# Kernel tuning notes

Hardware: AMD Instinct MI355X
Metric: run time of the kernel (lower is better)

Reference implementation:

```python
import jax, jax.numpy as jnp
import numpy as np

N, E, IN, HID, H, C, L, NC = 10000, 60000, 768, 256, 8, 256, 4, 2
EPS, SLOPE = 1e-5, 0.2

def _ln(x, g, b):
    m = x.mean(-1, keepdims=True)
    v = x.var(-1, keepdims=True)
    return (x - m) / jnp.sqrt(v + EPS) * g + b

def _gelu(x):
    return jax.nn.gelu(x, approximate=False)  # torch nn.GELU default (erf)

def setup_inputs() -> dict:
    key = jax.random.key(0)
    ks = iter(jax.random.split(key, 40))
    def p(shape, s=0.02):
        return jax.random.normal(next(ks), shape, jnp.float32) * s
    return dict(
        x=jax.random.normal(next(ks), (N, IN), jnp.float32),
        edge_index=jax.random.randint(next(ks), (2, E), 0, N, dtype=jnp.int32),
        W_in=p((HID, IN)), b_in=jnp.zeros((HID,), jnp.float32),
        virtual_node=p((1, HID)),
        Wl=p((L, H * C, HID)), bl=jnp.zeros((L, H * C), jnp.float32),
        Wr=p((L, H * C, HID)), br=jnp.zeros((L, H * C), jnp.float32),
        att=p((L, H, C)), gbias=jnp.zeros((L, HID), jnp.float32),
        V1=p((L, 2 * HID, HID)), v1b=jnp.zeros((L, 2 * HID), jnp.float32),
        V2=p((L, HID, 2 * HID)), v2b=jnp.zeros((L, HID), jnp.float32),
        U1=p((L, 2 * HID, 2 * HID)), u1b=jnp.zeros((L, 2 * HID), jnp.float32),
        U2=p((L, HID, 2 * HID)), u2b=jnp.zeros((L, HID), jnp.float32),
        g1=jnp.ones((L, HID), jnp.float32), be1=jnp.zeros((L, HID), jnp.float32),
        g2=jnp.ones((L, HID), jnp.float32), be2=jnp.zeros((L, HID), jnp.float32),
        g3=jnp.ones((L, HID), jnp.float32), be3=jnp.zeros((L, HID), jnp.float32),
        O1=p((HID, HID)), o1b=jnp.zeros((HID,), jnp.float32),
        O2=p((NC, HID)), o2b=jnp.zeros((NC,), jnp.float32),
    )

def reference(x, edge_index, W_in, b_in, virtual_node, Wl, bl, Wr, br, att, gbias,
              V1, v1b, V2, v2b, U1, u1b, U2, u2b,
              g1, be1, g2, be2, g3, be3, O1, o1b, O2, o2b):
    # add self loops (PyG add_self_loops=True)
    loops = jnp.arange(N, dtype=edge_index.dtype)
    src = jnp.concatenate([edge_index[0], loops])  # message sources j
    dst = jnp.concatenate([edge_index[1], loops])  # message targets i

    x = x @ W_in.T + b_in                      # [N, HID]
    vn = virtual_node                          # [1, HID]
    for i in range(L):
        # --- GATv2Conv (concat=False -> mean over heads), eval mode (no dropout) ---
        xl = (x @ Wl[i].T + bl[i]).reshape(N, H, C)   # source transform
        xr = (x @ Wr[i].T + br[i]).reshape(N, H, C)   # target transform
        m = jax.nn.leaky_relu(xl[src] + xr[dst], SLOPE)       # [Etot, H, C]
        e = jnp.einsum('ehc,hc->eh', m, att[i])                # [Etot, H]
        emax = jax.ops.segment_max(e, dst, num_segments=N)
        a = jnp.exp(e - emax[dst])
        denom = jax.ops.segment_sum(a, dst, num_segments=N)
        alpha = a / denom[dst]                                  # segment softmax
        agg = jax.ops.segment_sum(xl[src] * alpha[:, :, None], dst, num_segments=N)
        x_local = agg.mean(axis=1) + gbias[i]                   # [N, HID]
        x = _ln(x + x_local, g1[i], be1[i])
        # --- virtual node update ---
        vn_in = x.mean(axis=0, keepdims=True)
        vn_up = _gelu(vn_in @ V1[i].T + v1b[i]) @ V2[i].T + v2b[i]
        vn = _ln(vn + vn_up, g2[i], be2[i])
        # --- node update with broadcast VN ---
        xc = jnp.concatenate([x, jnp.broadcast_to(vn, (N, HID))], axis=1)
        xu = _gelu(xc @ U1[i].T + u1b[i]) @ U2[i].T + u2b[i]
        x = _ln(x + xu, g3[i], be3[i])
    return _gelu(x @ O1.T + o1b) @ O2.T + o2b
```

## Files before the change

### kernel.cpp

```cpp
#include <hip/hip_runtime.h>
#include <hip/hip_bf16.h>
#include <cstdint>
#include <cstddef>

#define N_NODES 10000
#define M_PAD   10112
#define N_EDGES 60000
#define ETOT    70000
#define DIM_IN  768
#define HID     256
#define NHEAD   8
#define CH      256
#define HC      2048
#define NLAYER  4
#define NCLS    2
#define EPSLN   1e-5f
#define SLOPE   0.2f
#define DEG_CAP 128

typedef __bf16 bf16;
typedef __bf16 bf16x8 __attribute__((ext_vector_type(8)));
typedef float  f32x4  __attribute__((ext_vector_type(4)));

__device__ __forceinline__ float gelu_erf(float x) {
  return 0.5f * x * (1.0f + erff(x * 0.70710678118654752f));
}

__device__ __forceinline__ void gl2lds16(const void* g, void* l) {
  __builtin_amdgcn_global_load_lds(
      (const __attribute__((address_space(1))) unsigned int*)g,
      (__attribute__((address_space(3))) unsigned int*)l,
      16, 0, 0);
}

__global__ void k_count(const int* __restrict__ ei, int* __restrict__ deg) {
  int e = blockIdx.x * 256 + threadIdx.x;
  if (e >= ETOT) return;
  int d = (e < N_EDGES) ? ei[N_EDGES + e] : (e - N_EDGES);
  atomicAdd(&deg[d], 1);
}

__global__ void k_scan(const int* __restrict__ deg, int* __restrict__ offs) {
  __shared__ int lds[1024];
  const int t = threadIdx.x;
  const int c0 = t * 10;
  int s = 0;
  #pragma unroll
  for (int q = 0; q < 10; ++q) { int idx = c0 + q; if (idx < N_NODES) s += deg[idx]; }
  lds[t] = s;
  __syncthreads();
  for (int o = 1; o < 1024; o <<= 1) {
    int v = (t >= o) ? lds[t - o] : 0;
    __syncthreads();
    lds[t] += v;
    __syncthreads();
  }
  int run = lds[t] - s;
  #pragma unroll
  for (int q = 0; q < 10; ++q) {
    int idx = c0 + q;
    if (idx < N_NODES) { offs[idx] = run; run += deg[idx]; }
  }
  if (t == 1023) offs[N_NODES] = lds[1023];
}

__global__ void k_scatter(const int* __restrict__ ei, const int* __restrict__ offs,
                          int* __restrict__ fill, int* __restrict__ adj) {
  int e = blockIdx.x * 256 + threadIdx.x;
  if (e >= ETOT) return;
  int s, d;
  if (e < N_EDGES) { s = ei[e]; d = ei[N_EDGES + e]; } else { s = e - N_EDGES; d = s; }
  int pos = offs[d] + atomicAdd(&fill[d], 1);
  adj[pos] = s;
}

__global__ void k_init_vn(const float* __restrict__ vnode, float* __restrict__ vn_cur) {
  int t = threadIdx.x;
  if (t < HID) vn_cur[t] = vnode[t];
}

__global__ void k_f2b(const float* __restrict__ src, bf16* __restrict__ dst, int n4) {
  int i = blockIdx.x * 256 + threadIdx.x;
  int stride = gridDim.x * 256;
  for (; i < n4; i += stride) {
    float4 v = reinterpret_cast<const float4*>(src)[i];
    bf16 o0 = (bf16)v.x, o1 = (bf16)v.y, o2 = (bf16)v.z, o3 = (bf16)v.w;
    ushort4 pack;
    pack.x = __builtin_bit_cast(unsigned short, o0);
    pack.y = __builtin_bit_cast(unsigned short, o1);
    pack.z = __builtin_bit_cast(unsigned short, o2);
    pack.w = __builtin_bit_cast(unsigned short, o3);
    reinterpret_cast<ushort4*>(dst)[i] = pack;
  }
}

__global__ void k_catw(const float* __restrict__ Wl, const float* __restrict__ Wr,
                       bf16* __restrict__ out) {
  int idx = blockIdx.x * 256 + threadIdx.x;
  const int total8 = NLAYER * 4096 * 256 / 8;
  if (idx >= total8) return;
  size_t flat = (size_t)idx * 8;
  int i   = (int)(flat / (4096 * 256));
  int rem = (int)(flat % (4096 * 256));
  int r = rem >> 8;
  int k = rem & 255;
  const float* src = (r < 2048)
      ? Wl + (((size_t)i * 2048 + r) << 8) + k
      : Wr + (((size_t)i * 2048 + (r - 2048)) << 8) + k;
  const float4* p4 = reinterpret_cast<const float4*>(src);
  float4 u0 = p4[0], u1 = p4[1];
  bf16x8 ov;
  ov[0]=(bf16)u0.x; ov[1]=(bf16)u0.y; ov[2]=(bf16)u0.z; ov[3]=(bf16)u0.w;
  ov[4]=(bf16)u1.x; ov[5]=(bf16)u1.y; ov[6]=(bf16)u1.z; ov[7]=(bf16)u1.w;
  reinterpret_cast<bf16x8*>(out)[idx] = ov;
}

__global__ void k_catb(const float* __restrict__ bl, const float* __restrict__ br,
                       float* __restrict__ out) {
  int idx = blockIdx.x * 256 + threadIdx.x;
  if (idx >= NLAYER * 4096) return;
  int i = idx >> 12, r = idx & 4095;
  out[idx] = (r < 2048) ? bl[i * 2048 + r] : br[i * 2048 + (r - 2048)];
}

template<int ACT, bool WB, bool WF>
__global__ __launch_bounds__(256) void k_gemm2(
    const bf16* __restrict__ A, int lda,
    const bf16* __restrict__ W, int ldw,
    const float* __restrict__ bias,
    bf16* __restrict__ Cb, float* __restrict__ Cf, int ldc,
    int M, int K)
{
  __shared__ bf16 As[128 * 64];
  __shared__ bf16 Bs[128 * 64];
  const int t = threadIdx.x;
  const int bm = blockIdx.x * 128;
  const int bn = blockIdx.y * 128;
  const int l = t & 63, w = t >> 6;
  const int wm = (w >> 1) * 64, wn = (w & 1) * 64;
  const int lr = l & 15, lg = l >> 4;
  const int sr = t >> 3;
  const int ps = t & 7;

  f32x4 acc[4][4];
  #pragma unroll
  for (int a = 0; a < 4; ++a)
    #pragma unroll
    for (int b = 0; b < 4; ++b) acc[a][b] = (f32x4){0.f, 0.f, 0.f, 0.f};

  for (int k0 = 0; k0 < K; k0 += 64) {
    #pragma unroll
    for (int q = 0; q < 4; ++q) {
      int r = q * 32 + sr;
      int ls = ps ^ (r & 7);
      gl2lds16(A + (size_t)(bm + r) * lda + k0 + ls * 8, &As[r * 64 + ps * 8]);
    }
    #pragma unroll
    for (int q = 0; q < 4; ++q) {
      int r = q * 32 + sr;
      int ls = ps ^ (r & 7);
      gl2lds16(W + (size_t)(bn + r) * ldw + k0 + ls * 8, &Bs[r * 64 + ps * 8]);
    }
    __syncthreads();
    #pragma unroll
    for (int ks = 0; ks < 2; ++ks) {
      bf16x8 af[4], bfr[4];
      #pragma unroll
      for (int mt = 0; mt < 4; ++mt) {
        int row = wm + mt * 16 + lr;
        int slot = ks * 4 + lg;
        af[mt] = *reinterpret_cast<const bf16x8*>(&As[row * 64 + ((slot ^ (row & 7)) * 8)]);
      }
      #pragma unroll
      for (int nt = 0; nt < 4; ++nt) {
        int row = wn + nt * 16 + lr;
        int slot = ks * 4 + lg;
        bfr[nt] = *reinterpret_cast<const bf16x8*>(&Bs[row * 64 + ((slot ^ (row & 7)) * 8)]);
      }
      #pragma unroll
      for (int mt = 0; mt < 4; ++mt)
        #pragma unroll
        for (int nt = 0; nt < 4; ++nt)
          acc[mt][nt] = __builtin_amdgcn_mfma_f32_16x16x32_bf16(af[mt], bfr[nt], acc[mt][nt], 0, 0, 0);
    }
    __syncthreads();
  }
  #pragma unroll
  for (int mt = 0; mt < 4; ++mt) {
    #pragma unroll
    for (int nt = 0; nt < 4; ++nt) {
      int col = bn + wn + nt * 16 + lr;
      float bv = bias[col];
      #pragma unroll
      for (int j = 0; j < 4; ++j) {
        int row = bm + wm + mt * 16 + lg * 4 + j;
        if (row < M) {
          float vv = acc[mt][nt][j] + bv;
          if (ACT == 1) vv = gelu_erf(vv);
          if (WB) Cb[(size_t)row * ldc + col] = (bf16)vv;
          if (WF) Cf[(size_t)row * ldc + col] = vv;
        }
      }
    }
  }
}

__global__ __launch_bounds__(256) void k_node_attn(
    float* __restrict__ x, bf16* __restrict__ xb,
    const bf16* __restrict__ xlr,
    const int* __restrict__ offs, const int* __restrict__ adj,
    const float* __restrict__ att_l, const float* __restrict__ gbias_l,
    const float* __restrict__ g_l, const float* __restrict__ b_l)
{
  __shared__ int   s_src[DEG_CAP];
  __shared__ float s_agg[HC];
  __shared__ float s_red[8];

  const int t = threadIdx.x;
  const int i = blockIdx.x;
  const int start = offs[i];
  int deg = offs[i + 1] - start;
  if (deg > DEG_CAP) deg = DEG_CAP;

  for (int j = t; j < deg; j += 256) s_src[j] = adj[start + j];

  float xr_reg[8], att_reg[8];
  {
    bf16x8 xv = *reinterpret_cast<const bf16x8*>(xlr + (size_t)i * 4096 + 2048 + 8 * t);
    #pragma unroll
    for (int q = 0; q < 8; ++q) xr_reg[q] = (float)xv[q];
    const float4* ap = reinterpret_cast<const float4*>(att_l + 8 * t);
    float4 a0 = ap[0], a1 = ap[1];
    att_reg[0]=a0.x; att_reg[1]=a0.y; att_reg[2]=a0.z; att_reg[3]=a0.w;
    att_reg[4]=a1.x; att_reg[5]=a1.y; att_reg[6]=a1.z; att_reg[7]=a1.w;
  }
  __syncthreads();

  float m = -1e30f, ssum = 0.f;
  float acc[8];
  #pragma unroll
  for (int q = 0; q < 8; ++q) acc[q] = 0.f;

  for (int j = 0; j < deg; ++j) {
    bf16x8 xv = *reinterpret_cast<const bf16x8*>(xlr + (size_t)s_src[j] * 4096 + 8 * t);
    float xf[8];
    float p = 0.f;
    #pragma unroll
    for (int q = 0; q < 8; ++q) {
      xf[q] = (float)xv[q];
      float z = xf[q] + xr_reg[q];
      z = (z > 0.f) ? z : SLOPE * z;
      p = fmaf(att_reg[q], z, p);
    }
    #pragma unroll
    for (int o = 16; o >= 1; o >>= 1) p += __shfl_xor(p, o, 32);
    if (__any(p > m)) {
      float mn = fmaxf(m, p);
      float scale = __expf(m - mn);
      ssum *= scale;
      #pragma unroll
      for (int q = 0; q < 8; ++q) acc[q] *= scale;
      m = mn;
    }
    float a = __expf(p - m);
    ssum += a;
    #pragma unroll
    for (int q = 0; q < 8; ++q) acc[q] = fmaf(a, xf[q], acc[q]);
  }
  float inv = 1.0f / ssum;
  #pragma unroll
  for (int q = 0; q < 8; ++q) s_agg[8 * t + q] = acc[q] * inv;
  __syncthreads();

  float xloc = 0.f;
  #pragma unroll
  for (int hh = 0; hh < NHEAD; ++hh) xloc += s_agg[hh * CH + t];
  xloc = xloc * (1.0f / NHEAD) + gbias_l[t];
  float r = x[(size_t)i * HID + t] + xloc;

  float s1 = r, s2 = r * r;
  #pragma unroll
  for (int o = 32; o >= 1; o >>= 1) { s1 += __shfl_xor(s1, o); s2 += __shfl_xor(s2, o); }
  if ((t & 63) == 0) { s_red[t >> 6] = s1; s_red[4 + (t >> 6)] = s2; }
  __syncthreads();
  s1 = s_red[0] + s_red[1] + s_red[2] + s_red[3];
  s2 = s_red[4] + s_red[5] + s_red[6] + s_red[7];
  float mean = s1 * (1.0f / HID);
  float var  = s2 * (1.0f / HID) - mean * mean;
  float o = (r - mean) * rsqrtf(var + EPSLN) * g_l[t] + b_l[t];
  x [(size_t)i * HID + t] = o;
  xb[(size_t)i * HID + t] = (bf16)o;
}

__global__ void k_colmean(const float* __restrict__ x, float* __restrict__ accum) {
  const int t = threadIdx.x, b = blockIdx.x;
  float s = 0.f;
  for (int r = b * 50; r < (b + 1) * 50; ++r) s += x[(size_t)r * HID + t];
  atomicAdd(&accum[t], s);
}

__global__ void k_vn_gemv1(const float* __restrict__ vn_accum,
                           const float* __restrict__ V1, const float* __restrict__ v1b,
                           float* __restrict__ z1) {
  const int o = blockIdx.x * 8 + (threadIdx.x >> 5);
  const int lane = threadIdx.x & 31;
  const float4* vp = reinterpret_cast<const float4*>(vn_accum + lane * 8);
  float4 a0 = vp[0], a1 = vp[1];
  const float4* wp = reinterpret_cast<const float4*>(V1 + (size_t)o * 256 + lane * 8);
  float4 w0 = wp[0], w1 = wp[1];
  float p = a0.x*w0.x + a0.y*w0.y + a0.z*w0.z + a0.w*w0.w
          + a1.x*w1.x + a1.y*w1.y + a1.z*w1.z + a1.w*w1.w;
  #pragma unroll
  for (int s = 16; s >= 1; s >>= 1) p += __shfl_xor(p, s, 32);
  if (lane == 0) z1[o] = gelu_erf(p * (1.0f / (float)N_NODES) + v1b[o]);
}

__global__ void k_vn_gemv2(const float* __restrict__ z1,
                           const float* __restrict__ V2, const float* __restrict__ v2b,
                           float* __restrict__ vn_up) {
  const int o = blockIdx.x * 8 + (threadIdx.x >> 5);
  const int lane = threadIdx.x & 31;
  float p = 0.f;
  #pragma unroll
  for (int c = 0; c < 4; ++c) {
    float4 a = reinterpret_cast<const float4*>(z1 + lane * 16)[c];
    float4 w = reinterpret_cast<const float4*>(V2 + (size_t)o * 512 + lane * 16)[c];
    p += a.x*w.x + a.y*w.y + a.z*w.z + a.w*w.w;
  }
  #pragma unroll
  for (int s = 16; s >= 1; s >>= 1) p += __shfl_xor(p, s, 32);
  if (lane == 0) vn_up[o] = p + v2b[o];
}

__global__ void k_vn_ln(float* __restrict__ vn_cur, const float* __restrict__ vn_up,
                        const float* __restrict__ g2, const float* __restrict__ be2) {
  __shared__ float s_red[8];
  const int t = threadIdx.x;
  float r = vn_cur[t] + vn_up[t];
  float s1 = r, s2 = r * r;
  #pragma unroll
  for (int o = 32; o >= 1; o >>= 1) { s1 += __shfl_xor(s1, o); s2 += __shfl_xor(s2, o); }
  if ((t & 63) == 0) { s_red[t >> 6] = s1; s_red[4 + (t >> 6)] = s2; }
  __syncthreads();
  s1 = s_red[0] + s_red[1] + s_red[2] + s_red[3];
  s2 = s_red[4] + s_red[5] + s_red[6] + s_red[7];
  float mean = s1 * (1.0f / HID);
  float var  = s2 * (1.0f / HID) - mean * mean;
  vn_cur[t] = (r - mean) * rsqrtf(var + EPSLN) * g2[t] + be2[t];
}

__global__ void k_vn_ctr(const float* __restrict__ vn_cur,
                         const float* __restrict__ U1, const float* __restrict__ u1b,
                         float* __restrict__ vn_ctr) {
  const int o = blockIdx.x * 8 + (threadIdx.x >> 5);
  const int lane = threadIdx.x & 31;
  const float4* vp = reinterpret_cast<const float4*>(vn_cur + lane * 8);
  float4 a0 = vp[0], a1 = vp[1];
  const float4* wp = reinterpret_cast<const float4*>(U1 + (size_t)o * 512 + 256 + lane * 8);
  float4 w0 = wp[0], w1 = wp[1];
  float p = a0.x*w0.x + a0.y*w0.y + a0.z*w0.z + a0.w*w0.w
          + a1.x*w1.x + a1.y*w1.y + a1.z*w1.z + a1.w*w1.w;
  #pragma unroll
  for (int s = 16; s >= 1; s >>= 1) p += __shfl_xor(p, s, 32);
  if (lane == 0) vn_ctr[o] = p + u1b[o];
}

__global__ __launch_bounds__(256) void k_ln_res(
    float* __restrict__ x, bf16* __restrict__ xb, const float* __restrict__ xu,
    const float* __restrict__ g_l, const float* __restrict__ b_l)
{
  __shared__ float s_red[8];
  const int t = threadIdx.x, i = blockIdx.x;
  float r = x[(size_t)i * HID + t] + xu[(size_t)i * HID + t];
  float s1 = r, s2 = r * r;
  #pragma unroll
  for (int o = 32; o >= 1; o >>= 1) { s1 += __shfl_xor(s1, o); s2 += __shfl_xor(s2, o); }
  if ((t & 63) == 0) { s_red[t >> 6] = s1; s_red[4 + (t >> 6)] = s2; }
  __syncthreads();
  s1 = s_red[0] + s_red[1] + s_red[2] + s_red[3];
  s2 = s_red[4] + s_red[5] + s_red[6] + s_red[7];
  float mean = s1 * (1.0f / HID);
  float var  = s2 * (1.0f / HID) - mean * mean;
  float o = (r - mean) * rsqrtf(var + EPSLN) * g_l[t] + b_l[t];
  x [(size_t)i * HID + t] = o;
  xb[(size_t)i * HID + t] = (bf16)o;
}

__global__ void k_final(const float* __restrict__ g, const float* __restrict__ O2,
                        const float* __restrict__ o2b, float* __restrict__ out) {
  int tid = blockIdx.x * 256 + threadIdx.x;
  if (tid >= N_NODES * NCLS) return;
  int n = tid >> 1, j = tid & 1;
  const float* gr = g + (size_t)n * HID;
  const float* w  = O2 + (size_t)j * HID;
  float d = o2b[j];
  for (int k = 0; k < HID; ++k) d = fmaf(gr[k], w[k], d);
  out[tid] = d;
}

extern "C" void kernel_launch(void* const* d_in, const int* in_sizes, int n_in,
                              void* d_out, int out_size, void* d_ws, size_t ws_size,
                              hipStream_t stream)
{
  const float* x_in  = (const float*)d_in[0];
  const int*   ei    = (const int*)  d_in[1];
  const float* W_in  = (const float*)d_in[2];
  const float* b_in  = (const float*)d_in[3];
  const float* vnode = (const float*)d_in[4];
  const float* Wl    = (const float*)d_in[5];
  const float* bl    = (const float*)d_in[6];
  const float* Wr    = (const float*)d_in[7];
  const float* br    = (const float*)d_in[8];
  const float* att   = (const float*)d_in[9];
  const float* gbias = (const float*)d_in[10];
  const float* V1    = (const float*)d_in[11];
  const float* v1b   = (const float*)d_in[12];
  const float* V2    = (const float*)d_in[13];
  const float* v2b   = (const float*)d_in[14];
  const float* U1    = (const float*)d_in[15];
  const float* u1b   = (const float*)d_in[16];
  const float* U2    = (const float*)d_in[17];
  const float* u2b   = (const float*)d_in[18];
  const float* g1    = (const float*)d_in[19];
  const float* be1   = (const float*)d_in[20];
  const float* g2    = (const float*)d_in[21];
  const float* be2   = (const float*)d_in[22];
  const float* g3    = (const float*)d_in[23];
  const float* be3   = (const float*)d_in[24];
  const float* O1    = (const float*)d_in[25];
  const float* o1b   = (const float*)d_in[26];
  const float* O2    = (const float*)d_in[27];
  const float* o2b   = (const float*)d_in[28];
  float* out = (float*)d_out;

  char* ws = (char*)d_ws;
  size_t cur = 0;
  auto alloc = [&](size_t bytes) -> char* {
    char* p = ws + cur;
    cur = (cur + bytes + 255) & ~(size_t)255;
    return p;
  };
  float* x        = (float*)alloc((size_t)M_PAD * HID * 4);
  bf16*  xb       = (bf16*) alloc((size_t)M_PAD * HID * 2);
  bf16*  xlr      = (bf16*) alloc((size_t)M_PAD * 4096 * 2);
  bf16*  h1       = (bf16*) alloc((size_t)M_PAD * 2 * HID * 2);
  float* xu       = (float*)alloc((size_t)M_PAD * HID * 4);
  bf16*  Wlrb     = (bf16*) alloc((size_t)NLAYER * 4096 * HID * 2);
  float* blr      = (float*)alloc((size_t)NLAYER * 4096 * 4);
  bf16*  U1b      = (bf16*) alloc((size_t)NLAYER * 2 * HID * 2 * HID * 2);
  bf16*  U2b      = (bf16*) alloc((size_t)NLAYER * HID * 2 * HID * 2);
  bf16*  O1b      = (bf16*) alloc((size_t)HID * HID * 2);
  bf16*  Winb     = (bf16*) alloc((size_t)HID * DIM_IN * 2);
  int*   deg      = (int*)  alloc((size_t)N_NODES * 4);
  int*   offs     = (int*)  alloc((size_t)(N_NODES + 1) * 4);
  int*   fill     = (int*)  alloc((size_t)N_NODES * 4);
  int*   adj      = (int*)  alloc((size_t)ETOT * 4);
  float* vn_accum = (float*)alloc(HID * 4);
  float* vn_cur   = (float*)alloc(HID * 4);
  float* vn_ctr   = (float*)alloc(2 * HID * 4);
  float* z1buf    = (float*)alloc(2 * HID * 4);
  float* vn_up    = (float*)alloc(HID * 4);

  bf16* x_in_b = xlr;

  hipMemsetAsync(deg, 0, (size_t)N_NODES * 4, stream);
  hipMemsetAsync(fill, 0, (size_t)N_NODES * 4, stream);
  k_count<<<(ETOT + 255) / 256, 256, 0, stream>>>(ei, deg);
  k_scan<<<1, 1024, 0, stream>>>(deg, offs);
  k_scatter<<<(ETOT + 255) / 256, 256, 0, stream>>>(ei, offs, fill, adj);
  k_init_vn<<<1, 256, 0, stream>>>(vnode, vn_cur);

  k_catw<<<(NLAYER * 4096 * 256 / 8 + 255) / 256, 256, 0, stream>>>(Wl, Wr, Wlrb);
  k_catb<<<(NLAYER * 4096 + 255) / 256, 256, 0, stream>>>(bl, br, blr);
  k_f2b<<<256, 256, 0, stream>>>(U1, U1b, NLAYER * 2 * HID * 2 * HID / 4);
  k_f2b<<<128, 256, 0, stream>>>(U2, U2b, NLAYER * HID * 2 * HID / 4);
  k_f2b<<<64, 256, 0, stream>>>(O1, O1b, HID * HID / 4);
  k_f2b<<<64, 256, 0, stream>>>(W_in, Winb, HID * DIM_IN / 4);
  k_f2b<<<512, 256, 0, stream>>>(x_in, x_in_b, N_NODES * DIM_IN / 4);

  {
    dim3 g(M_PAD / 128, HID / 128);
    k_gemm2<0, true, true><<<g, 256, 0, stream>>>(
        x_in_b, DIM_IN, Winb, DIM_IN, b_in, xb, x, HID, N_NODES, DIM_IN);
  }

  dim3 g_proj(M_PAD / 128, 4096 / 128);
  dim3 g_u1  (M_PAD / 128, (2 * HID) / 128);
  dim3 g_u2  (M_PAD / 128, HID / 128);

  for (int i = 0; i < NLAYER; ++i) {
    const bf16* Wlrb_i = Wlrb + (size_t)i * 4096 * HID;
    const bf16* U1b_i  = U1b + (size_t)i * 2 * HID * 2 * HID;
    const bf16* U2b_i  = U2b + (size_t)i * HID * 2 * HID;

    k_gemm2<0, true, false><<<g_proj, 256, 0, stream>>>(
        xb, HID, Wlrb_i, HID, blr + (size_t)i * 4096, xlr, nullptr, 4096, N_NODES, HID);

    k_node_attn<<<N_NODES, 256, 0, stream>>>(x, xb, xlr, offs, adj,
        att + (size_t)i * HC, gbias + (size_t)i * HID,
        g1 + (size_t)i * HID, be1 + (size_t)i * HID);

    hipMemsetAsync(vn_accum, 0, HID * 4, stream);
    k_colmean<<<200, 256, 0, stream>>>(x, vn_accum);
    k_vn_gemv1<<<64, 256, 0, stream>>>(vn_accum,
        V1 + (size_t)i * 2 * HID * HID, v1b + (size_t)i * 2 * HID, z1buf);
    k_vn_gemv2<<<32, 256, 0, stream>>>(z1buf,
        V2 + (size_t)i * HID * 2 * HID, v2b + (size_t)i * HID, vn_up);
    k_vn_ln<<<1, 256, 0, stream>>>(vn_cur, vn_up,
        g2 + (size_t)i * HID, be2 + (size_t)i * HID);
    k_vn_ctr<<<64, 256, 0, stream>>>(vn_cur,
        U1 + (size_t)i * 2 * HID * 2 * HID, u1b + (size_t)i * 2 * HID, vn_ctr);

    k_gemm2<1, true, false><<<g_u1, 256, 0, stream>>>(
        xb, HID, U1b_i, 2 * HID, vn_ctr, h1, nullptr, 2 * HID, N_NODES, HID);
    k_gemm2<0, false, true><<<g_u2, 256, 0, stream>>>(
        h1, 2 * HID, U2b_i, 2 * HID, u2b + (size_t)i * HID, nullptr, xu, HID, N_NODES, 2 * HID);

    k_ln_res<<<N_NODES, 256, 0, stream>>>(x, xb, xu, g3 + (size_t)i * HID, be3 + (size_t)i * HID);
  }

  k_gemm2<1, false, true><<<g_u2, 256, 0, stream>>>(
      xb, HID, O1b, HID, o1b, nullptr, xu, HID, N_NODES, HID);
  k_final<<<(N_NODES * NCLS + 255) / 256, 256, 0, stream>>>(xu, O2, o2b, out);
}
```

Measured before the change: 1.034 ms.

## Double-buffer GEMM LDS tiles and remap workgroups across XCDs

New measurement: 971.9 us. -6.0%, faster.

```diff
diff --git a/kernel.cpp b/kernel.cpp
--- a/kernel.cpp
+++ b/kernel.cpp
@@ -129,13 +129,18 @@
     const bf16* __restrict__ W, int ldw,
     const float* __restrict__ bias,
     bf16* __restrict__ Cb, float* __restrict__ Cf, int ldc,
-    int M, int K)
+    int M, int K, int NT)
 {
-  __shared__ bf16 As[128 * 64];
-  __shared__ bf16 Bs[128 * 64];
+  __shared__ bf16 As[2][128 * 64];
+  __shared__ bf16 Bs[2][128 * 64];
   const int t = threadIdx.x;
-  const int bm = blockIdx.x * 128;
-  const int bn = blockIdx.y * 128;
+  const int nwg = gridDim.x;
+  const int qq = nwg >> 3, rr = nwg & 7;
+  const int xcd = blockIdx.x & 7, loc = blockIdx.x >> 3;
+  const int wg = (xcd < rr) ? (xcd * (qq + 1) + loc)
+                            : (rr * (qq + 1) + (xcd - rr) * qq + loc);
+  const int bm = (wg / NT) * 128;
+  const int bn = (wg % NT) * 128;
   const int l = t & 63, w = t >> 6;
   const int wm = (w >> 1) * 64, wn = (w & 1) * 64;
   const int lr = l & 15, lg = l >> 4;
@@ -148,20 +153,28 @@
     #pragma unroll
     for (int b = 0; b < 4; ++b) acc[a][b] = (f32x4){0.f, 0.f, 0.f, 0.f};
 
-  for (int k0 = 0; k0 < K; k0 += 64) {
+  auto stage = [&](int buf, int k0) {
     #pragma unroll
     for (int q = 0; q < 4; ++q) {
       int r = q * 32 + sr;
       int ls = ps ^ (r & 7);
-      gl2lds16(A + (size_t)(bm + r) * lda + k0 + ls * 8, &As[r * 64 + ps * 8]);
+      gl2lds16(A + (size_t)(bm + r) * lda + k0 + ls * 8, &As[buf][r * 64 + ps * 8]);
     }
     #pragma unroll
     for (int q = 0; q < 4; ++q) {
       int r = q * 32 + sr;
       int ls = ps ^ (r & 7);
-      gl2lds16(W + (size_t)(bn + r) * ldw + k0 + ls * 8, &Bs[r * 64 + ps * 8]);
+      gl2lds16(W + (size_t)(bn + r) * ldw + k0 + ls * 8, &Bs[buf][r * 64 + ps * 8]);
     }
-    __syncthreads();
+  };
+
+  const int nt = K >> 6;
+  stage(0, 0);
+  __syncthreads();
+  for (int kt = 0; kt < nt; ++kt) {
+    if (kt + 1 < nt) stage((kt + 1) & 1, (kt + 1) << 6);
+    const bf16* Ab = As[kt & 1];
+    const bf16* Bb = Bs[kt & 1];
     #pragma unroll
     for (int ks = 0; ks < 2; ++ks) {
       bf16x8 af[4], bfr[4];
@@ -169,33 +182,33 @@
       for (int mt = 0; mt < 4; ++mt) {
         int row = wm + mt * 16 + lr;
         int slot = ks * 4 + lg;
-        af[mt] = *reinterpret_cast<const bf16x8*>(&As[row * 64 + ((slot ^ (row & 7)) * 8)]);
+        af[mt] = *reinterpret_cast<const bf16x8*>(&Ab[row * 64 + ((slot ^ (row & 7)) * 8)]);
       }
       #pragma unroll
-      for (int nt = 0; nt < 4; ++nt) {
-        int row = wn + nt * 16 + lr;
+      for (int nt2 = 0; nt2 < 4; ++nt2) {
+        int row = wn + nt2 * 16 + lr;
         int slot = ks * 4 + lg;
-        bfr[nt] = *reinterpret_cast<const bf16x8*>(&Bs[row * 64 + ((slot ^ (row & 7)) * 8)]);
+        bfr[nt2] = *reinterpret_cast<const bf16x8*>(&Bb[row * 64 + ((slot ^ (row & 7)) * 8)]);
       }
       #pragma unroll
       for (int mt = 0; mt < 4; ++mt)
         #pragma unroll
-        for (int nt = 0; nt < 4; ++nt)
-          acc[mt][nt] = __builtin_amdgcn_mfma_f32_16x16x32_bf16(af[mt], bfr[nt], acc[mt][nt], 0, 0, 0);
+        for (int nt2 = 0; nt2 < 4; ++nt2)
+          acc[mt][nt2] = __builtin_amdgcn_mfma_f32_16x16x32_bf16(af[mt], bfr[nt2], acc[mt][nt2], 0, 0, 0);
     }
     __syncthreads();
   }
   #pragma unroll
   for (int mt = 0; mt < 4; ++mt) {
     #pragma unroll
-    for (int nt = 0; nt < 4; ++nt) {
-      int col = bn + wn + nt * 16 + lr;
+    for (int nt2 = 0; nt2 < 4; ++nt2) {
+      int col = bn + wn + nt2 * 16 + lr;
       float bv = bias[col];
       #pragma unroll
       for (int j = 0; j < 4; ++j) {
         int row = bm + wm + mt * 16 + lg * 4 + j;
         if (row < M) {
-          float vv = acc[mt][nt][j] + bv;
+          float vv = acc[mt][nt2][j] + bv;
           if (ACT == 1) vv = gelu_erf(vv);
           if (WB) Cb[(size_t)row * ldc + col] = (bf16)vv;
           if (WF) Cf[(size_t)row * ldc + col] = vv;
@@ -478,23 +491,18 @@
   k_f2b<<<64, 256, 0, stream>>>(W_in, Winb, HID * DIM_IN / 4);
   k_f2b<<<512, 256, 0, stream>>>(x_in, x_in_b, N_NODES * DIM_IN / 4);
 
-  {
-    dim3 g(M_PAD / 128, HID / 128);
-    k_gemm2<0, true, true><<<g, 256, 0, stream>>>(
-        x_in_b, DIM_IN, Winb, DIM_IN, b_in, xb, x, HID, N_NODES, DIM_IN);
-  }
-
-  dim3 g_proj(M_PAD / 128, 4096 / 128);
-  dim3 g_u1  (M_PAD / 128, (2 * HID) / 128);
-  dim3 g_u2  (M_PAD / 128, HID / 128);
+  const int MT = M_PAD / 128;
+
+  k_gemm2<0, true, true><<<MT * 2, 256, 0, stream>>>(
+      x_in_b, DIM_IN, Winb, DIM_IN, b_in, xb, x, HID, N_NODES, DIM_IN, 2);
 
   for (int i = 0; i < NLAYER; ++i) {
     const bf16* Wlrb_i = Wlrb + (size_t)i * 4096 * HID;
     const bf16* U1b_i  = U1b + (size_t)i * 2 * HID * 2 * HID;
     const bf16* U2b_i  = U2b + (size_t)i * HID * 2 * HID;
 
-    k_gemm2<0, true, false><<<g_proj, 256, 0, stream>>>(
-        xb, HID, Wlrb_i, HID, blr + (size_t)i * 4096, xlr, nullptr, 4096, N_NODES, HID);
+    k_gemm2<0, true, false><<<MT * 32, 256, 0, stream>>>(
+        xb, HID, Wlrb_i, HID, blr + (size_t)i * 4096, xlr, nullptr, 4096, N_NODES, HID, 32);
 
     k_node_attn<<<N_NODES, 256, 0, stream>>>(x, xb, xlr, offs, adj,
         att + (size_t)i * HC, gbias + (size_t)i * HID,
@@ -511,15 +519,15 @@
     k_vn_ctr<<<64, 256, 0, stream>>>(vn_cur,
         U1 + (size_t)i * 2 * HID * 2 * HID, u1b + (size_t)i * 2 * HID, vn_ctr);
 
-    k_gemm2<1, true, false><<<g_u1, 256, 0, stream>>>(
-        xb, HID, U1b_i, 2 * HID, vn_ctr, h1, nullptr, 2 * HID, N_NODES, HID);
-    k_gemm2<0, false, true><<<g_u2, 256, 0, stream>>>(
-        h1, 2 * HID, U2b_i, 2 * HID, u2b + (size_t)i * HID, nullptr, xu, HID, N_NODES, 2 * HID);
+    k_gemm2<1, true, false><<<MT * 4, 256, 0, stream>>>(
+        xb, HID, U1b_i, 2 * HID, vn_ctr, h1, nullptr, 2 * HID, N_NODES, HID, 4);
+    k_gemm2<0, false, true><<<MT * 2, 256, 0, stream>>>(
+        h1, 2 * HID, U2b_i, 2 * HID, u2b + (size_t)i * HID, nullptr, xu, HID, N_NODES, 2 * HID, 2);
 
     k_ln_res<<<N_NODES, 256, 0, stream>>>(x, xb, xu, g3 + (size_t)i * HID, be3 + (size_t)i * HID);
   }
 
-  k_gemm2<1, false, true><<<g_u2, 256, 0, stream>>>(
-      xb, HID, O1b, HID, o1b, nullptr, xu, HID, N_NODES, HID);
+  k_gemm2<1, false, true><<<MT * 2, 256, 0, stream>>>(
+      xb, HID, O1b, HID, o1b, nullptr, xu, HID, N_NODES, HID, 2);
   k_final<<<(N_NODES * NCLS + 255) / 256, 256, 0, stream>>>(xu, O2, o2b, out);
 }
```
